# Performance work log

Measured on AMD Instinct MI355X. Metric: run time of the kernel, lower is better.

The kernel has to match this reference:

```python
import jax, jax.numpy as jnp
import numpy as np

D = 2048
N = 16384
ETA = 0.01


def setup_inputs() -> dict:
    key = jax.random.key(0)
    k_theta, k_xs = jax.random.split(key)
    theta = jax.random.normal(k_theta, (D,), dtype=jnp.float32)
    # per-layer params x_k, init uniform(-1/sqrt(d), 1/sqrt(d)) as in torch module
    stdv = 1.0 / np.sqrt(D)
    xs = jax.random.uniform(k_xs, (N, D), dtype=jnp.float32, minval=-stdv, maxval=stdv)
    return {"theta": theta, "xs": xs}


def reference(theta, xs):
    # Each layer: pred = <x, theta>; grad = -x / (1 + exp(pred));
    # theta_next = theta - eta * grad = theta + eta * x / (1 + exp(pred)).
    def step(th, x):
        pred = jnp.dot(x, th)
        th_next = th + ETA * x / (1.0 + jnp.exp(pred))
        return th_next, None

    theta_out, _ = jax.lax.scan(step, theta, xs)
    return theta_out
```

## Files before the change

### kernel.cpp

```cpp
#include <hip/hip_runtime.h>
#include <hip/hip_bf16.h>
#include <stdint.h>

#define D_DIM 2048
#define N_STEPS 16384
#define B_BLK 1024
#define N_BLK (N_STEPS / B_BLK)
#define T_P (B_BLK / 128)
#define N_TILE (T_P * (T_P + 1) / 2)
#define ETA 0.01f
#define NWG 256
#define FLAG_STRIDE 16

typedef __attribute__((ext_vector_type(8))) short short8_t;
typedef __attribute__((ext_vector_type(4))) float floatx4;

__device__ __forceinline__ short f2bf(float f) {
  __hip_bfloat16 h = __float2bfloat16(f);
  return __builtin_bit_cast(short, h);
}
__device__ __forceinline__ float bf2f(uint32_t bits) {
  return __builtin_bit_cast(float, bits << 16);
}

__device__ __forceinline__ void store_wt(float* p, float v) {
  __hip_atomic_store(p, v, __ATOMIC_RELAXED, __HIP_MEMORY_SCOPE_AGENT);
}

__device__ __forceinline__ void gl_lds16(const short* g, short* l) {
  __builtin_amdgcn_global_load_lds(
      (const __attribute__((address_space(1))) void*)g,
      (__attribute__((address_space(3))) void*)l, 16, 0, 0);
}

__global__ __launch_bounds__(256) void cast_kernel(const float* __restrict__ xs,
                                                   short* __restrict__ xb) {
  size_t i = (size_t)blockIdx.x * 256 + threadIdx.x;
  float4 a = ((const float4*)xs)[i * 2];
  float4 b = ((const float4*)xs)[i * 2 + 1];
  short8_t v;
  v[0] = f2bf(a.x); v[1] = f2bf(a.y); v[2] = f2bf(a.z); v[3] = f2bf(a.w);
  v[4] = f2bf(b.x); v[5] = f2bf(b.y); v[6] = f2bf(b.z); v[7] = f2bf(b.w);
  *(short8_t*)(xb + i * 8) = v;
}

__global__ __launch_bounds__(256) void gram_kernel(const short* __restrict__ xb,
                                                   short* __restrict__ G) {
  int i = blockIdx.x;
  int x = i & 7, j = i >> 3;
  int b = (j < 36) ? x : x + 8;
  int t = (j < 36) ? j : j - 36;
  int ti = 0;
  while ((ti + 1) * (ti + 2) / 2 <= t) ti++;
  int tj = t - ti * (ti + 1) / 2;

  __shared__ short As[128 * 64];
  __shared__ short Bs[128 * 64];

  int tid = threadIdx.x;
  int lane = tid & 63;
  int w = tid >> 6;
  int wm = w >> 1, wn = w & 1;
  int quad = lane >> 4, rr = lane & 15;

  floatx4 acc[4][4];
#pragma unroll
  for (int ii = 0; ii < 4; ii++)
#pragma unroll
    for (int jj = 0; jj < 4; jj++)
#pragma unroll
      for (int r = 0; r < 4; r++) acc[ii][jj][r] = 0.f;

  const short* Arow = xb + (size_t)(b * B_BLK + ti * 128) * D_DIM;
  const short* Brow = xb + (size_t)(b * B_BLK + tj * 128) * D_DIM;
  bool diag = (ti == tj);

  for (int kk = 0; kk < D_DIM; kk += 64) {
#pragma unroll
    for (int tch = 0; tch < 4; tch++) {
      int chunk = tch * 256 + tid;
      int row = chunk >> 3, slot = chunk & 7;
      int cc = slot ^ (row & 7);
      gl_lds16(Arow + (size_t)row * D_DIM + kk + cc * 8, &As[chunk * 8]);
      if (!diag)
        gl_lds16(Brow + (size_t)row * D_DIM + kk + cc * 8, &Bs[chunk * 8]);
    }
    __syncthreads();

    const short* Bsrc = diag ? As : Bs;
#pragma unroll
    for (int ks = 0; ks < 2; ks++) {
      short8_t af[4], bfr[4];
#pragma unroll
      for (int mt = 0; mt < 4; mt++) {
        int r = wm * 64 + mt * 16 + rr;
        int slot = (ks * 4 + quad) ^ (r & 7);
        af[mt] = *(const short8_t*)(&As[r * 64 + slot * 8]);
      }
#pragma unroll
      for (int nt = 0; nt < 4; nt++) {
        int r = wn * 64 + nt * 16 + rr;
        int slot = (ks * 4 + quad) ^ (r & 7);
        bfr[nt] = *(const short8_t*)(&Bsrc[r * 64 + slot * 8]);
      }
#pragma unroll
      for (int mt = 0; mt < 4; mt++)
#pragma unroll
        for (int nt = 0; nt < 4; nt++)
          acc[mt][nt] = __builtin_amdgcn_mfma_f32_16x16x32_bf16(
              af[mt], bfr[nt], acc[mt][nt], 0, 0, 0);
    }
    __syncthreads();
  }

  size_t gbase = ((size_t)(b * N_TILE + t)) * (128 * 128);
  int col0 = lane & 15;
  int row0 = (lane >> 4) * 4;
#pragma unroll
  for (int mt = 0; mt < 4; mt++)
#pragma unroll
    for (int nt = 0; nt < 4; nt++)
#pragma unroll
      for (int r = 0; r < 4; r++) {
        int row = wm * 64 + mt * 16 + row0 + r;
        int col = wn * 64 + nt * 16 + col0;
        G[gbase + (size_t)row * 128 + col] = f2bf(acc[mt][nt][r]);
      }
}

__device__ __forceinline__ void grid_barrier(int* flags, int* release, int gen,
                                             int wg, int tid) {
  __syncthreads();
  if (wg == 0) {
    if (tid > 0) {
      int guard = 0;
      while (__hip_atomic_load(&flags[tid * FLAG_STRIDE], __ATOMIC_RELAXED,
                               __HIP_MEMORY_SCOPE_AGENT) < gen &&
             guard < (1 << 20)) {
        guard++;
        __builtin_amdgcn_s_sleep(1);
      }
    }
    __syncthreads();
    if (tid == 0)
      __hip_atomic_store(release, gen, __ATOMIC_RELAXED,
                         __HIP_MEMORY_SCOPE_AGENT);
  } else {
    if (tid == 0) {
      __hip_atomic_store(&flags[wg * FLAG_STRIDE], gen, __ATOMIC_RELAXED,
                         __HIP_MEMORY_SCOPE_AGENT);
      int guard = 0;
      while (__hip_atomic_load(release, __ATOMIC_RELAXED,
                               __HIP_MEMORY_SCOPE_AGENT) < gen &&
             guard < (1 << 20)) {
        guard++;
        __builtin_amdgcn_s_sleep(1);
      }
    }
  }
  asm volatile("" ::: "memory");
  __syncthreads();
}

__device__ __forceinline__ float wave_reduce(float s) {
  for (int off = 32; off; off >>= 1) s += __shfl_xor(s, off, 64);
  return s;
}

__global__ __launch_bounds__(256, 1) void solve_kernel(
    const short* __restrict__ xb, const short* __restrict__ G,
    float* __restrict__ theta_arr, float* __restrict__ c0_arr,
    float* __restrict__ c1_arr, int* flags, int* release) {
  int tid = threadIdx.x;
  int wg = blockIdx.x;
  int lane = tid & 63;
  int wid = tid >> 6;
  int gw = wg * 4 + wid;
  int gen = 0;

  __shared__ float c1s[B_BLK];
  __shared__ float redc[4][4][8];

  for (int b = 0; b < N_BLK; b++) {
    const float* theta = theta_arr + (size_t)b * D_DIM;
    float* c0 = c0_arr + (size_t)b * B_BLK;
    float* c1 = c1_arr + (size_t)b * B_BLK;
    float p_k;

    {
      const short* xr = xb + (size_t)(b * B_BLK + gw) * D_DIM;
      float s = 0.f;
#pragma unroll
      for (int i = 0; i < 4; i++) {
        int idx = (i * 64 + lane) * 8;
        short8_t xv = *(const short8_t*)(xr + idx);
        float4 t0 = *(const float4*)(theta + idx);
        float4 t1 = *(const float4*)(theta + idx + 4);
        s += bf2f((uint16_t)xv[0]) * t0.x + bf2f((uint16_t)xv[1]) * t0.y +
             bf2f((uint16_t)xv[2]) * t0.z + bf2f((uint16_t)xv[3]) * t0.w +
             bf2f((uint16_t)xv[4]) * t1.x + bf2f((uint16_t)xv[5]) * t1.y +
             bf2f((uint16_t)xv[6]) * t1.z + bf2f((uint16_t)xv[7]) * t1.w;
      }
      s = wave_reduce(s);
      p_k = s;
      if (lane == 0) store_wt(&c0[gw], ETA / (1.f + __expf(s)));
    }
    grid_barrier(flags, release, ++gen, wg, tid);

    {
      int ti = gw >> 7, kr = gw & 127;
      float s = 0.f;
      for (int tj = 0; tj <= ti; tj++) {
        size_t base =
            ((size_t)(b * N_TILE + ti * (ti + 1) / 2 + tj)) * (128 * 128) +
            (size_t)kr * 128;
        uint32_t gv = *(const uint32_t*)(G + base + lane * 2);
        float2 cv = *(const float2*)(c0 + tj * 128 + lane * 2);
        int jc = lane * 2;
        int lim = (tj == ti) ? kr : 128;
        if (jc < lim) s += bf2f(gv & 0xffffu) * cv.x;
        if (jc + 1 < lim) s += bf2f(gv >> 16) * cv.y;
      }
      s = wave_reduce(s);
      if (lane == 0) store_wt(&c1[gw], ETA / (1.f + __expf(p_k + s)));
    }
    grid_barrier(flags, release, ++gen, wg, tid);

    if (wg < 64) {
#pragma unroll
      for (int i = 0; i < 4; i++) c1s[i * 256 + tid] = c1[i * 256 + tid];
      __syncthreads();
      int d0 = wg * 32;
      const short* xp =
          xb + (size_t)(b * B_BLK) * D_DIM + d0 + (lane & 3) * 8;
      float a8[8] = {0.f, 0.f, 0.f, 0.f, 0.f, 0.f, 0.f, 0.f};
      int rbase = wid * 256 + (lane >> 2);
      for (int i = 0; i < 16; i++) {
        int row = rbase + i * 16;
        short8_t xv = *(const short8_t*)(xp + (size_t)row * D_DIM);
        float c = c1s[row];
#pragma unroll
        for (int jj = 0; jj < 8; jj++) a8[jj] += c * bf2f((uint16_t)xv[jj]);
      }
#pragma unroll
      for (int off = 4; off < 64; off <<= 1)
#pragma unroll
        for (int jj = 0; jj < 8; jj++) a8[jj] += __shfl_xor(a8[jj], off, 64);
      if (lane < 4) {
#pragma unroll
        for (int jj = 0; jj < 8; jj++) redc[wid][lane][jj] = a8[jj];
      }
      __syncthreads();
      if (tid < 32) {
        int oct = tid >> 3, e = tid & 7;
        float tot = redc[0][oct][e] + redc[1][oct][e] + redc[2][oct][e] +
                    redc[3][oct][e];
        store_wt(&theta_arr[(size_t)(b + 1) * D_DIM + d0 + tid],
                 theta[d0 + tid] + tot);
      }
    }
    if (b < N_BLK - 1) grid_barrier(flags, release, ++gen, wg, tid);
  }
}

extern "C" void kernel_launch(void* const* d_in, const int* in_sizes, int n_in,
                              void* d_out, int out_size, void* d_ws,
                              size_t ws_size, hipStream_t stream) {
  const float* theta_in = (const float*)d_in[0];
  const float* xs = (const float*)d_in[1];

  char* ws = (char*)d_ws;
  const size_t XB_BYTES = (size_t)N_STEPS * D_DIM * sizeof(short);
  const size_t G_BYTES = (size_t)N_BLK * N_TILE * 128 * 128 * sizeof(short);
  short* xb = (short*)ws;
  short* G = (short*)(ws + XB_BYTES);
  float* theta_arr = (float*)(ws + XB_BYTES + G_BYTES);
  float* c0_arr = theta_arr + (size_t)(N_BLK + 1) * D_DIM;
  float* c1_arr = c0_arr + (size_t)N_BLK * B_BLK;
  int* flags = (int*)(c1_arr + (size_t)N_BLK * B_BLK);
  int* release = flags + NWG * FLAG_STRIDE;

  hipMemsetAsync(flags, 0, (NWG * FLAG_STRIDE + 16) * sizeof(int), stream);
  hipMemcpyAsync(theta_arr, theta_in, D_DIM * sizeof(float),
                 hipMemcpyDeviceToDevice, stream);

  cast_kernel<<<(N_STEPS * D_DIM / 8) / 256, 256, 0, stream>>>(xs, xb);
  gram_kernel<<<N_BLK * N_TILE, 256, 0, stream>>>(xb, G);
  solve_kernel<<<NWG, 256, 0, stream>>>(xb, G, theta_arr, c0_arr, c1_arr,
                                        flags, release);

  hipMemcpyAsync(d_out, theta_arr + (size_t)N_BLK * D_DIM,
                 D_DIM * sizeof(float), hipMemcpyDeviceToDevice, stream);
}
```

Measured before the change: 438.4 us.

## Replace centralized grid barrier with all-to-all flags and prefetch loads across barriers

Replaces the coordinator-based grid barrier (workgroup 0 polls and then releases) with split arrive/wait phases. Each workgroup publishes its own flag and its threads poll all 256 flags directly, which removes the extra release round-trip. Global loads of x rows, G tiles and x columns for the next phase are issued between arrive and wait, so memory latency overlaps the barrier. The theta-update phase is spread over all 256 workgroups instead of 64, with 8 output columns each. In exchange there is more polling traffic (256 loads per workgroup per barrier) and more registers held for the prefetched data.

```diff
diff --git a/kernel.cpp b/kernel.cpp
--- a/kernel.cpp
+++ b/kernel.cpp
@@ -128,35 +128,21 @@
       }
 }
 
-__device__ __forceinline__ void grid_barrier(int* flags, int* release, int gen,
-                                             int wg, int tid) {
+__device__ __forceinline__ void bar_arrive(int* flags, int wg, int tid,
+                                           int gen) {
   __syncthreads();
-  if (wg == 0) {
-    if (tid > 0) {
-      int guard = 0;
-      while (__hip_atomic_load(&flags[tid * FLAG_STRIDE], __ATOMIC_RELAXED,
-                               __HIP_MEMORY_SCOPE_AGENT) < gen &&
-             guard < (1 << 20)) {
-        guard++;
-        __builtin_amdgcn_s_sleep(1);
-      }
-    }
-    __syncthreads();
-    if (tid == 0)
-      __hip_atomic_store(release, gen, __ATOMIC_RELAXED,
-                         __HIP_MEMORY_SCOPE_AGENT);
-  } else {
-    if (tid == 0) {
-      __hip_atomic_store(&flags[wg * FLAG_STRIDE], gen, __ATOMIC_RELAXED,
-                         __HIP_MEMORY_SCOPE_AGENT);
-      int guard = 0;
-      while (__hip_atomic_load(release, __ATOMIC_RELAXED,
-                               __HIP_MEMORY_SCOPE_AGENT) < gen &&
-             guard < (1 << 20)) {
-        guard++;
-        __builtin_amdgcn_s_sleep(1);
-      }
-    }
+  if (tid == 0)
+    __hip_atomic_store(&flags[wg * FLAG_STRIDE], gen, __ATOMIC_RELAXED,
+                       __HIP_MEMORY_SCOPE_AGENT);
+}
+
+__device__ __forceinline__ void bar_wait(int* flags, int tid, int gen) {
+  int guard = 0;
+  while (__hip_atomic_load(&flags[tid * FLAG_STRIDE], __ATOMIC_RELAXED,
+                           __HIP_MEMORY_SCOPE_AGENT) < gen &&
+         guard < (1 << 20)) {
+    guard++;
+    __builtin_amdgcn_s_sleep(1);
   }
   asm volatile("" ::: "memory");
   __syncthreads();
@@ -176,26 +162,48 @@
   int lane = tid & 63;
   int wid = tid >> 6;
   int gw = wg * 4 + wid;
+  int ti = gw >> 7, kr = gw & 127;
+  int oct = (wg & 7) * 32 + (wg >> 3);
+  int d0 = oct * 8;
   int gen = 0;
-
-  __shared__ float c1s[B_BLK];
-  __shared__ float redc[4][4][8];
+  (void)release;
+
+  __shared__ float redc[4][8];
+
+  short8_t xa[4];
+  uint32_t gv[8];
+  short8_t xc[4];
+
+  {
+    const short* xr = xb + (size_t)gw * D_DIM;
+#pragma unroll
+    for (int i = 0; i < 4; i++)
+      xa[i] = *(const short8_t*)(xr + (i * 64 + lane) * 8);
+#pragma unroll
+    for (int tj = 0; tj < T_P; tj++)
+      if (tj <= ti) {
+        size_t base = ((size_t)(ti * (ti + 1) / 2 + tj)) * (128 * 128) +
+                      (size_t)kr * 128;
+        gv[tj] = *(const uint32_t*)(G + base + lane * 2);
+      }
+  }
 
   for (int b = 0; b < N_BLK; b++) {
     const float* theta = theta_arr + (size_t)b * D_DIM;
     float* c0 = c0_arr + (size_t)b * B_BLK;
     float* c1 = c1_arr + (size_t)b * B_BLK;
     float p_k;
+    float th8 = 0.f;
 
     {
-      const short* xr = xb + (size_t)(b * B_BLK + gw) * D_DIM;
+      if (tid < 8) th8 = theta[d0 + tid];
       float s = 0.f;
 #pragma unroll
       for (int i = 0; i < 4; i++) {
         int idx = (i * 64 + lane) * 8;
-        short8_t xv = *(const short8_t*)(xr + idx);
         float4 t0 = *(const float4*)(theta + idx);
         float4 t1 = *(const float4*)(theta + idx + 4);
+        short8_t xv = xa[i];
         s += bf2f((uint16_t)xv[0]) * t0.x + bf2f((uint16_t)xv[1]) * t0.y +
              bf2f((uint16_t)xv[2]) * t0.z + bf2f((uint16_t)xv[3]) * t0.w +
              bf2f((uint16_t)xv[4]) * t1.x + bf2f((uint16_t)xv[5]) * t1.y +
@@ -205,61 +213,82 @@
       p_k = s;
       if (lane == 0) store_wt(&c0[gw], ETA / (1.f + __expf(s)));
     }
-    grid_barrier(flags, release, ++gen, wg, tid);
-
+    bar_arrive(flags, wg, tid, ++gen);
     {
-      int ti = gw >> 7, kr = gw & 127;
+      const short* xp = xb + ((size_t)b * B_BLK + tid * 4) * D_DIM + d0;
+#pragma unroll
+      for (int j = 0; j < 4; j++)
+        xc[j] = *(const short8_t*)(xp + (size_t)j * D_DIM);
+    }
+    bar_wait(flags, tid, gen);
+
+    {
+      float2 cv[T_P];
+#pragma unroll
+      for (int tj = 0; tj < T_P; tj++)
+        if (tj <= ti) cv[tj] = *(const float2*)(c0 + tj * 128 + lane * 2);
       float s = 0.f;
-      for (int tj = 0; tj <= ti; tj++) {
-        size_t base =
-            ((size_t)(b * N_TILE + ti * (ti + 1) / 2 + tj)) * (128 * 128) +
-            (size_t)kr * 128;
-        uint32_t gv = *(const uint32_t*)(G + base + lane * 2);
-        float2 cv = *(const float2*)(c0 + tj * 128 + lane * 2);
-        int jc = lane * 2;
-        int lim = (tj == ti) ? kr : 128;
-        if (jc < lim) s += bf2f(gv & 0xffffu) * cv.x;
-        if (jc + 1 < lim) s += bf2f(gv >> 16) * cv.y;
-      }
+      int jc = lane * 2;
+#pragma unroll
+      for (int tj = 0; tj < T_P; tj++)
+        if (tj <= ti) {
+          int lim = (tj == ti) ? kr : 128;
+          if (jc < lim) s += bf2f(gv[tj] & 0xffffu) * cv[tj].x;
+          if (jc + 1 < lim) s += bf2f(gv[tj] >> 16) * cv[tj].y;
+        }
       s = wave_reduce(s);
       if (lane == 0) store_wt(&c1[gw], ETA / (1.f + __expf(p_k + s)));
     }
-    grid_barrier(flags, release, ++gen, wg, tid);
-
-    if (wg < 64) {
-#pragma unroll
-      for (int i = 0; i < 4; i++) c1s[i * 256 + tid] = c1[i * 256 + tid];
+    bar_arrive(flags, wg, tid, ++gen);
+    if (b + 1 < N_BLK) {
+      const short* xr = xb + (size_t)((b + 1) * B_BLK + gw) * D_DIM;
+#pragma unroll
+      for (int i = 0; i < 4; i++)
+        xa[i] = *(const short8_t*)(xr + (i * 64 + lane) * 8);
+    }
+    bar_wait(flags, tid, gen);
+
+    {
+      float4 c1v = *(const float4*)(c1 + tid * 4);
+      float a8[8];
+#pragma unroll
+      for (int jj = 0; jj < 8; jj++) a8[jj] = 0.f;
+#pragma unroll
+      for (int j = 0; j < 4; j++) {
+        float c = (&c1v.x)[j];
+        short8_t xv = xc[j];
+#pragma unroll
+        for (int jj = 0; jj < 8; jj++) a8[jj] += c * bf2f((uint16_t)xv[jj]);
+      }
+#pragma unroll
+      for (int off = 32; off; off >>= 1)
+#pragma unroll
+        for (int jj = 0; jj < 8; jj++) a8[jj] += __shfl_xor(a8[jj], off, 64);
+      if (lane == 0) {
+#pragma unroll
+        for (int jj = 0; jj < 8; jj++) redc[wid][jj] = a8[jj];
+      }
       __syncthreads();
-      int d0 = wg * 32;
-      const short* xp =
-          xb + (size_t)(b * B_BLK) * D_DIM + d0 + (lane & 3) * 8;
-      float a8[8] = {0.f, 0.f, 0.f, 0.f, 0.f, 0.f, 0.f, 0.f};
-      int rbase = wid * 256 + (lane >> 2);
-      for (int i = 0; i < 16; i++) {
-        int row = rbase + i * 16;
-        short8_t xv = *(const short8_t*)(xp + (size_t)row * D_DIM);
-        float c = c1s[row];
-#pragma unroll
-        for (int jj = 0; jj < 8; jj++) a8[jj] += c * bf2f((uint16_t)xv[jj]);
-      }
-#pragma unroll
-      for (int off = 4; off < 64; off <<= 1)
-#pragma unroll
-        for (int jj = 0; jj < 8; jj++) a8[jj] += __shfl_xor(a8[jj], off, 64);
-      if (lane < 4) {
-#pragma unroll
-        for (int jj = 0; jj < 8; jj++) redc[wid][lane][jj] = a8[jj];
-      }
-      __syncthreads();
-      if (tid < 32) {
-        int oct = tid >> 3, e = tid & 7;
-        float tot = redc[0][oct][e] + redc[1][oct][e] + redc[2][oct][e] +
-                    redc[3][oct][e];
-        store_wt(&theta_arr[(size_t)(b + 1) * D_DIM + d0 + tid],
-                 theta[d0 + tid] + tot);
-      }
-    }
-    if (b < N_BLK - 1) grid_barrier(flags, release, ++gen, wg, tid);
+      if (tid < 8) {
+        float tot =
+            redc[0][tid] + redc[1][tid] + redc[2][tid] + redc[3][tid];
+        store_wt(&theta_arr[(size_t)(b + 1) * D_DIM + d0 + tid], th8 + tot);
+      }
+    }
+    if (b + 1 < N_BLK) {
+      bar_arrive(flags, wg, tid, ++gen);
+      {
+        size_t base =
+            ((size_t)((b + 1) * N_TILE + ti * (ti + 1) / 2)) * (128 * 128) +
+            (size_t)kr * 128;
+#pragma unroll
+        for (int tj = 0; tj < T_P; tj++)
+          if (tj <= ti)
+            gv[tj] = *(const uint32_t*)(G + base + (size_t)tj * (128 * 128) +
+                                        lane * 2);
+      }
+      bar_wait(flags, tid, gen);
+    }
   }
 }
 
```

Measured after the change: 353.2 us. 19.4% less time.
